# Kernel optimization log

Hardware: AMD Instinct MI355X
Metric: run time of the kernel (lower is better)

Reference implementation:

```python
import jax, jax.numpy as jnp
import numpy as np

HIDDEN = 1024
HEADS = 16
HEAD_DIM = HIDDEN // HEADS  # 64; softmax scale uses head_dim per SeqAttention(hidden_size=head_dim)


def setup_inputs() -> dict:
    key = jax.random.key(0)
    ks = jax.random.split(key, 7)
    B, M = 2, 2048
    s = 1.0 / np.sqrt(HIDDEN)
    return {
        "query": jax.random.normal(ks[0], (B, M, HIDDEN), jnp.float32),
        "key": jax.random.normal(ks[1], (B, M, HIDDEN), jnp.float32),
        "value": jax.random.normal(ks[2], (B, M, HIDDEN), jnp.float32),
        "Wq": jax.random.normal(ks[3], (HIDDEN, HIDDEN), jnp.float32) * s,
        "Wk": jax.random.normal(ks[4], (HIDDEN, HIDDEN), jnp.float32) * s,
        "Wv": jax.random.normal(ks[5], (HIDDEN, HIDDEN), jnp.float32) * s,
        "Wo": jax.random.normal(ks[6], (HIDDEN, HIDDEN), jnp.float32) * s,
    }


def _split_heads(x):
    # [B, T, H*D] -> [B, H, T, D]
    B, T, _ = x.shape
    return x.reshape(B, T, HEADS, HEAD_DIM).transpose(0, 2, 1, 3)


def reference(query, key, value, Wq, Wk, Wv, Wo):
    # nn.Linear(bias=False): y = x @ W.T
    q = _split_heads(query @ Wq.T)  # [B,H,M,D]
    k = _split_heads(key @ Wk.T)    # [B,H,N,D]
    v = _split_heads(value @ Wv.T)  # [B,H,N,D]
    scale = 1.0 / jnp.sqrt(jnp.asarray(HEAD_DIM, q.dtype))
    attn = jnp.einsum("bhmd,bhnd->bhmn", q, k) * scale
    attn = jax.nn.softmax(attn, axis=-1)
    out = jnp.einsum("bhmn,bhnd->bhmd", attn, v)  # [B,H,M,D]
    B, H, M, D = out.shape
    out = out.transpose(0, 2, 1, 3).reshape(B, M, H * D)
    return out @ Wo.T
```

## Files before the change

kernel.cpp:

```cpp
#include <hip/hip_runtime.h>

typedef __bf16 bf16;
typedef __bf16 bf16x2 __attribute__((ext_vector_type(2)));
typedef __bf16 bf16x8 __attribute__((ext_vector_type(8)));
typedef float  f32x4  __attribute__((ext_vector_type(4)));
typedef float  f32x16 __attribute__((ext_vector_type(16)));
typedef unsigned int u32;
typedef unsigned int u32x4 __attribute__((ext_vector_type(4)));

typedef __attribute__((address_space(1))) unsigned int gu32;
typedef __attribute__((address_space(3))) unsigned int lu32;

__device__ __forceinline__ void llds16(const void* g, void* l) {
  __builtin_amdgcn_global_load_lds((gu32*)g, (lu32*)l, 16, 0, 0);
}

__device__ __forceinline__ void cvt8(const float* __restrict__ src,
                                     bf16* __restrict__ dst, int i) {
  const float4* s4 = (const float4*)src;
  float4 a = s4[i * 2 + 0];
  float4 c = s4[i * 2 + 1];
  bf16x8 o;
  o[0] = (bf16)a.x; o[1] = (bf16)a.y; o[2] = (bf16)a.z; o[3] = (bf16)a.w;
  o[4] = (bf16)c.x; o[5] = (bf16)c.y; o[6] = (bf16)c.z; o[7] = (bf16)c.w;
  ((bf16x8*)dst)[i] = o;
}

__global__ __launch_bounds__(256) void cvt_bf16(const float* __restrict__ src,
                                                bf16* __restrict__ dst, int n8) {
  int i = blockIdx.x * blockDim.x + threadIdx.x;
  if (i < n8) cvt8(src, dst, i);
}

__global__ __launch_bounds__(256) void cvt_all(const float* __restrict__ w0,
                                               const float* __restrict__ w1,
                                               const float* __restrict__ w2,
                                               const float* __restrict__ w3,
                                               const float* __restrict__ x0,
                                               const float* __restrict__ x1,
                                               const float* __restrict__ x2,
                                               bf16* __restrict__ wdst,
                                               bf16* __restrict__ xdst) {
  const int b = blockIdx.x;
  if (b < 2048) {
    const int which = b >> 9;
    const float* src = (which == 0) ? w0 : (which == 1) ? w1 : (which == 2) ? w2 : w3;
    const int i = (b & 511) * 256 + threadIdx.x;
    cvt8(src, wdst + (size_t)which * (1u << 20), i);
  } else {
    const int b2 = b - 2048;
    const int which = b2 >> 11;
    const float* src = (which == 0) ? x0 : (which == 1) ? x1 : x2;
    const int i = (b2 & 2047) * 256 + threadIdx.x;
    cvt8(src, xdst + (size_t)which * (4u << 20), i);
  }
}

__global__ __launch_bounds__(256) void gemm_qkv(const bf16* __restrict__ A0,
                                                const bf16* __restrict__ A1,
                                                const bf16* __restrict__ A2,
                                                const bf16* __restrict__ Wb,
                                                bf16* __restrict__ qb,
                                                bf16* __restrict__ kb,
                                                bf16* __restrict__ vb,
                                                int zoff) {
  constexpr int K = 1024, BM = 128, BN = 128, BK = 32, NT = K / BK;
  __shared__ bf16 Alds[2][BM * BK];
  __shared__ bf16 Blds[2][BN * BK];
  const int t = threadIdx.x, w = t >> 6, l = t & 63;
  const int lr = l & 15, lg = l >> 4;
  const int bm = blockIdx.x * BM, bn = blockIdx.y * BN;
  const int z = blockIdx.z + zoff;
  const bf16* A = (z == 0) ? A0 : (z == 1) ? A1 : A2;
  const bf16* W = Wb + (size_t)z * (1u << 20);
  const int wm = (w >> 1) * 64, wn = (w & 1) * 64;

  f32x4 acc[4][4] = {};

  auto stage = [&](int buf, int kt) {
    const int k0 = kt * BK;
#pragma unroll
    for (int i = 0; i < 2; ++i) {
      int idx = i * 256 + t;
      int row = idx >> 2, kb2 = (idx & 3) * 16;
      llds16((const char*)A + ((size_t)(bm + row) * K + k0) * 2 + kb2,
             (char*)(&Alds[buf][0]) + (i * 4 + w) * 1024);
    }
#pragma unroll
    for (int i = 0; i < 2; ++i) {
      int idx = i * 256 + t;
      int row = idx >> 2, kb2 = (idx & 3) * 16;
      llds16((const char*)W + ((size_t)(bn + row) * K + k0) * 2 + kb2,
             (char*)(&Blds[buf][0]) + (i * 4 + w) * 1024);
    }
  };

  stage(0, 0);
  for (int kt = 0; kt < NT; ++kt) {
    __syncthreads();
    if (kt + 1 < NT) stage((kt + 1) & 1, kt + 1);
    const int cur = kt & 1;
    bf16x8 af[4], bfr[4];
#pragma unroll
    for (int i = 0; i < 4; ++i)
      af[i] = *(const bf16x8*)(&Alds[cur][(wm + i * 16 + lr) * BK + lg * 8]);
#pragma unroll
    for (int j = 0; j < 4; ++j)
      bfr[j] = *(const bf16x8*)(&Blds[cur][(wn + j * 16 + lr) * BK + lg * 8]);
    __builtin_amdgcn_s_setprio(1);
#pragma unroll
    for (int i = 0; i < 4; ++i)
#pragma unroll
      for (int j = 0; j < 4; ++j)
        acc[i][j] = __builtin_amdgcn_mfma_f32_16x16x32_bf16(af[i], bfr[j], acc[i][j], 0, 0, 0);
    __builtin_amdgcn_s_setprio(0);
  }

  bf16* Cout = (z == 0) ? qb : (z == 1) ? kb : vb;
  const float osc = (z == 0) ? 0.1803368801f : 1.0f;
#pragma unroll
  for (int i = 0; i < 4; ++i) {
#pragma unroll
    for (int j = 0; j < 4; ++j) {
#pragma unroll
      for (int r = 0; r < 4; ++r) {
        const int gm = bm + wm + i * 16 + lg * 4 + r;
        const int n  = bn + wn + j * 16 + lr;
        const int b = gm >> 11, m = gm & 2047;
        const int h = n >> 6, d = n & 63;
        const size_t off = (z < 2)
            ? ((size_t)((b * 16 + h) * 2048 + m) * 64 + d)
            : ((size_t)((b * 16 + h) * 64 + d) * 2048 + m);
        Cout[off] = (bf16)(acc[i][j][r] * osc);
      }
    }
  }
}

__global__ __launch_bounds__(256) void gemm_out(const bf16* __restrict__ A,
                                                const bf16* __restrict__ Bw,
                                                float* __restrict__ Cout) {
  constexpr int N = 1024, K = 1024;
  constexpr int BM = 128, BN = 64, BK = 32;
  __shared__ bf16 Alds[2][BM * BK];
  __shared__ bf16 Blds[2][BN * BK];
  const int t = threadIdx.x;
  const int w = t >> 6, l = t & 63;
  const int lr = l & 15, lg = l >> 4;
  const int bm = blockIdx.x * BM, bn = blockIdx.y * BN;
  const int wm = (w >> 1) * 64, wn = (w & 1) * 32;

  f32x4 acc[4][2] = {};

  auto stage = [&](int buf, int kt) {
    const int k0 = kt * BK;
#pragma unroll
    for (int i = 0; i < 2; ++i) {
      int idx = i * 256 + t;
      int row = idx >> 2, kb = (idx & 3) * 16;
      const char* g = (const char*)A + ((size_t)(bm + row) * K + k0) * 2 + kb;
      llds16(g, (char*)(&Alds[buf][0]) + (i * 4 + w) * 1024);
    }
    {
      int row = t >> 2, kb = (t & 3) * 16;
      const char* g = (const char*)Bw + ((size_t)(bn + row) * K + k0) * 2 + kb;
      llds16(g, (char*)(&Blds[buf][0]) + w * 1024);
    }
  };

  stage(0, 0);
  constexpr int NT = K / BK;
  for (int kt = 0; kt < NT; ++kt) {
    __syncthreads();
    if (kt + 1 < NT) stage((kt + 1) & 1, kt + 1);
    const int cur = kt & 1;
    bf16x8 af[4], bfr[2];
#pragma unroll
    for (int i = 0; i < 4; ++i)
      af[i] = *(const bf16x8*)(&Alds[cur][(wm + i * 16 + lr) * BK + lg * 8]);
#pragma unroll
    for (int j = 0; j < 2; ++j)
      bfr[j] = *(const bf16x8*)(&Blds[cur][(wn + j * 16 + lr) * BK + lg * 8]);
    __builtin_amdgcn_s_setprio(1);
#pragma unroll
    for (int i = 0; i < 4; ++i)
#pragma unroll
      for (int j = 0; j < 2; ++j)
        acc[i][j] = __builtin_amdgcn_mfma_f32_16x16x32_bf16(af[i], bfr[j], acc[i][j], 0, 0, 0);
    __builtin_amdgcn_s_setprio(0);
  }

#pragma unroll
  for (int i = 0; i < 4; ++i)
#pragma unroll
    for (int j = 0; j < 2; ++j)
#pragma unroll
      for (int r = 0; r < 4; ++r) {
        const int gm = bm + wm + i * 16 + lg * 4 + r;
        const int n  = bn + wn + j * 16 + lr;
        Cout[(size_t)gm * N + n] = acc[i][j][r];
      }
}

__global__ __launch_bounds__(256) void attn_fwd(const bf16* __restrict__ Qb,
                                                const bf16* __restrict__ Kb,
                                                const bf16* __restrict__ Vt,
                                                bf16* __restrict__ Out) {
  constexpr int Mlen = 2048, KVB = 64, NTT = Mlen / KVB;
  __shared__ bf16 Klds[3][KVB * 64];
  __shared__ bf16 Vlds[3][64 * KVB];
  const int t = threadIdx.x, w = t >> 6, l = t & 63;
  const int l31 = l & 31, hi = l >> 5;
  const int orig = blockIdx.x;
  const int wg = (orig & 7) * 64 + (orig >> 3);
  const int bh = wg >> 4;
  const int qr = (wg & 15) * 128 + w * 32;
  const int key = (l31 & 7) << 4;

  const bf16* qbase = Qb + ((size_t)bh * Mlen + qr + l31) * 64;
  bf16x8 qf[4];
#pragma unroll
  for (int dks = 0; dks < 4; ++dks)
    qf[dks] = *(const bf16x8*)(qbase + dks * 16 + hi * 8);

  f32x16 acco0 = {}, acco1 = {};
  float lsum = 0.f;

  const char* kTile0 = (const char*)Kb + (size_t)bh * Mlen * 64 * 2;
  const char* vBase  = (const char*)Vt + (size_t)bh * 64 * Mlen * 2;

  auto stageKV = [&](int buf, int tile) {
    const int kv0 = tile * KVB;
#pragma unroll
    for (int i = 0; i < 2; ++i) {
      int idx = i * 256 + t;
      int L = idx * 16;
      int row = L >> 7;
      int inner = (L & 127) ^ ((row & 7) << 4);
      llds16(kTile0 + (size_t)(kv0 + row) * 128 + inner,
             (char*)(&Klds[buf][0]) + (i * 4 + w) * 1024);
    }
#pragma unroll
    for (int i = 0; i < 2; ++i) {
      int idx = i * 256 + t;
      int L = idx * 16;
      int d = L >> 7;
      int inner = (L & 127) ^ ((d & 7) << 4);
      llds16(vBase + (size_t)d * (Mlen * 2) + kv0 * 2 + inner,
             (char*)(&Vlds[buf][0]) + (i * 4 + w) * 1024);
    }
  };

  stageKV(0, 0);
  int bufc = 0;
  for (int tile = 0; tile < NTT; ++tile) {
    const int bufn = (bufc == 2) ? 0 : bufc + 1;
    if (tile + 1 < NTT) {
      stageKV(bufn, tile + 1);
      asm volatile("s_waitcnt vmcnt(4)" ::: "memory");
    } else {
      asm volatile("s_waitcnt vmcnt(0)" ::: "memory");
    }
    __builtin_amdgcn_s_barrier();
    __builtin_amdgcn_sched_barrier(0);
    const char* kb_ = (const char*)(&Klds[bufc][0]);
    const char* vb_ = (const char*)(&Vlds[bufc][0]);

    f32x16 s0 = {}, s1 = {};
    __builtin_amdgcn_s_setprio(1);
#pragma unroll
    for (int dks = 0; dks < 4; ++dks) {
      const int a0 = (0 * 32 + l31) * 128 + ((dks * 32 + hi * 16) ^ key);
      const int a1 = (1 * 32 + l31) * 128 + ((dks * 32 + hi * 16) ^ key);
      bf16x8 kf0 = *(const bf16x8*)(kb_ + a0);
      bf16x8 kf1 = *(const bf16x8*)(kb_ + a1);
      s0 = __builtin_amdgcn_mfma_f32_32x32x16_bf16(kf0, qf[dks], s0, 0, 0, 0);
      s1 = __builtin_amdgcn_mfma_f32_32x32x16_bf16(kf1, qf[dks], s1, 0, 0, 0);
    }
    __builtin_amdgcn_s_setprio(0);

    u32 wrd0[8], wrd1[8];
    float ts = 0.f;
#pragma unroll
    for (int e2 = 0; e2 < 8; ++e2) {
      const float p00 = __builtin_amdgcn_exp2f(s0[2 * e2]);
      const float p01 = __builtin_amdgcn_exp2f(s0[2 * e2 + 1]);
      const float p10 = __builtin_amdgcn_exp2f(s1[2 * e2]);
      const float p11 = __builtin_amdgcn_exp2f(s1[2 * e2 + 1]);
      ts += (p00 + p01) + (p10 + p11);
      bf16x2 k0; k0[0] = (bf16)p00; k0[1] = (bf16)p01;
      bf16x2 k1; k1[0] = (bf16)p10; k1[1] = (bf16)p11;
      wrd0[e2] = __builtin_bit_cast(u32, k0);
      wrd1[e2] = __builtin_bit_cast(u32, k1);
    }
    lsum += ts;

    __builtin_amdgcn_s_setprio(1);
#pragma unroll
    for (int ks = 0; ks < 2; ++ks) {
      auto sa0 = __builtin_amdgcn_permlane32_swap(wrd0[4 * ks + 0], wrd0[4 * ks + 2], false, false);
      auto sa1 = __builtin_amdgcn_permlane32_swap(wrd0[4 * ks + 1], wrd0[4 * ks + 3], false, false);
      auto sb0 = __builtin_amdgcn_permlane32_swap(wrd1[4 * ks + 0], wrd1[4 * ks + 2], false, false);
      auto sb1 = __builtin_amdgcn_permlane32_swap(wrd1[4 * ks + 1], wrd1[4 * ks + 3], false, false);
      u32x4 fa, fb;
      fa[0] = (u32)sa0[0]; fa[1] = (u32)sa1[0]; fa[2] = (u32)sa0[1]; fa[3] = (u32)sa1[1];
      fb[0] = (u32)sb0[0]; fb[1] = (u32)sb1[0]; fb[2] = (u32)sb0[1]; fb[3] = (u32)sb1[1];
      const bf16x8 pa = __builtin_bit_cast(bf16x8, fa);
      const bf16x8 pb = __builtin_bit_cast(bf16x8, fb);
      const int c0 = (ks * 32 + hi * 16);
      bf16x8 va0 = *(const bf16x8*)(vb_ + (0 * 32 + l31) * 128 + ((0 * 64 + c0) ^ key));
      bf16x8 va1 = *(const bf16x8*)(vb_ + (1 * 32 + l31) * 128 + ((0 * 64 + c0) ^ key));
      bf16x8 vb0 = *(const bf16x8*)(vb_ + (0 * 32 + l31) * 128 + ((1 * 64 + c0) ^ key));
      bf16x8 vb1 = *(const bf16x8*)(vb_ + (1 * 32 + l31) * 128 + ((1 * 64 + c0) ^ key));
      acco0 = __builtin_amdgcn_mfma_f32_32x32x16_bf16(pa, va0, acco0, 0, 0, 0);
      acco1 = __builtin_amdgcn_mfma_f32_32x32x16_bf16(pa, va1, acco1, 0, 0, 0);
      acco0 = __builtin_amdgcn_mfma_f32_32x32x16_bf16(pb, vb0, acco0, 0, 0, 0);
      acco1 = __builtin_amdgcn_mfma_f32_32x32x16_bf16(pb, vb1, acco1, 0, 0, 0);
    }
    __builtin_amdgcn_s_setprio(0);
    bufc = bufn;
  }

  float lf = lsum + __shfl_xor(lsum, 32, 64);
  const float inv = 1.0f / lf;
  const int b = bh >> 4, h = bh & 15;
#pragma unroll
  for (int e = 0; e < 16; ++e) {
    const int ql = (e & 3) + 8 * (e >> 2) + 4 * hi;
    const float iv = __shfl(inv, ql, 64);
    const size_t row = (size_t)(b * 2048 + qr + ql) * 1024 + h * 64;
    Out[row + l31]      = (bf16)(acco0[e] * iv);
    Out[row + 32 + l31] = (bf16)(acco1[e] * iv);
  }
}

extern "C" void kernel_launch(void* const* d_in, const int* in_sizes, int n_in,
                              void* d_out, int out_size, void* d_ws, size_t ws_size,
                              hipStream_t stream) {
  const float* q  = (const float*)d_in[0];
  const float* k  = (const float*)d_in[1];
  const float* v  = (const float*)d_in[2];
  const float* Wq = (const float*)d_in[3];
  const float* Wk = (const float*)d_in[4];
  const float* Wv = (const float*)d_in[5];
  const float* Wo = (const float*)d_in[6];

  char* ws = (char*)d_ws;
  const dim3 cb(256);

  if (ws_size >= ((size_t)56 << 20)) {
    bf16* Wb = (bf16*)ws;
    bf16* Xq = (bf16*)(ws + (8u  << 20));
    bf16* Xk = (bf16*)(ws + (16u << 20));
    bf16* Xv = (bf16*)(ws + (24u << 20));
    bf16* qb = (bf16*)(ws + (32u << 20));
    bf16* kb = (bf16*)(ws + (40u << 20));
    bf16* vb = (bf16*)(ws + (48u << 20));
    bf16* Xa = (bf16*)(ws + (8u  << 20));

    cvt_all<<<8192, cb, 0, stream>>>(Wq, Wk, Wv, Wo, q, k, v, Wb, Xq);
    gemm_qkv<<<dim3(32, 8, 3), cb, 0, stream>>>(Xq, Xk, Xv, Wb, qb, kb, vb, 0);
    attn_fwd<<<512, cb, 0, stream>>>(qb, kb, vb, Xa);
    gemm_out<<<dim3(32, 16), cb, 0, stream>>>(Xa, Wb + 3 * (1u << 20), (float*)d_out);
  } else {
    bf16* Wb = (bf16*)ws;
    bf16* X  = (bf16*)(ws + (8u  << 20));
    bf16* qb = (bf16*)(ws + (16u << 20));
    bf16* kb = (bf16*)(ws + (24u << 20));
    bf16* vb = (bf16*)(ws + (32u << 20));
    bf16* Xa = (bf16*)(ws + (8u  << 20));

    cvt_all<<<2048, cb, 0, stream>>>(Wq, Wk, Wv, Wo, q, k, v, Wb, Wb);
    cvt_bf16<<<2048, cb, 0, stream>>>(q, X, 524288);
    gemm_qkv<<<dim3(32, 8, 1), cb, 0, stream>>>(X, X, X, Wb, qb, kb, vb, 0);
    cvt_bf16<<<2048, cb, 0, stream>>>(k, X, 524288);
    gemm_qkv<<<dim3(32, 8, 1), cb, 0, stream>>>(X, X, X, Wb, qb, kb, vb, 1);
    cvt_bf16<<<2048, cb, 0, stream>>>(v, X, 524288);
    gemm_qkv<<<dim3(32, 8, 1), cb, 0, stream>>>(X, X, X, Wb, qb, kb, vb, 2);
    attn_fwd<<<512, cb, 0, stream>>>(qb, kb, vb, Xa);
    gemm_out<<<dim3(32, 16), cb, 0, stream>>>(Xa, Wb + 3 * (1u << 20), (float*)d_out);
  }
}
```

Measured before the change: 131.8 us.

## Pre-swizzle V into MFMA fragment layout and load from global, row sums via MFMA

```diff
diff --git a/kernel.cpp b/kernel.cpp
--- a/kernel.cpp
+++ b/kernel.cpp
@@ -128,9 +128,17 @@
         const int n  = bn + wn + j * 16 + lr;
         const int b = gm >> 11, m = gm & 2047;
         const int h = n >> 6, d = n & 63;
-        const size_t off = (z < 2)
-            ? ((size_t)((b * 16 + h) * 2048 + m) * 64 + d)
-            : ((size_t)((b * 16 + h) * 64 + d) * 2048 + m);
+        size_t off;
+        if (z < 2) {
+          off = (size_t)((b * 16 + h) * 2048 + m) * 64 + d;
+        } else {
+          const int tile = m >> 6, kvb = (m >> 5) & 1, kss = (m >> 4) & 1;
+          const int hii = (m >> 3) & 1, jj = m & 7;
+          const int vblk = d >> 5, dl = d & 31;
+          off = (size_t)(b * 16 + h) * 131072 +
+                (size_t)(((tile * 4 + kvb * 2 + kss) * 2 + vblk) * 512 +
+                         (hii * 32 + dl) * 8 + jj);
+        }
         Cout[off] = (bf16)(acc[i][j][r] * osc);
       }
     }
@@ -207,8 +215,7 @@
                                                 const bf16* __restrict__ Vt,
                                                 bf16* __restrict__ Out) {
   constexpr int Mlen = 2048, KVB = 64, NTT = Mlen / KVB;
-  __shared__ bf16 Klds[3][KVB * 64];
-  __shared__ bf16 Vlds[3][64 * KVB];
+  __shared__ bf16 Klds[2][KVB * 64];
   const int t = threadIdx.x, w = t >> 6, l = t & 63;
   const int l31 = l & 31, hi = l >> 5;
   const int orig = blockIdx.x;
@@ -223,13 +230,18 @@
   for (int dks = 0; dks < 4; ++dks)
     qf[dks] = *(const bf16x8*)(qbase + dks * 16 + hi * 8);
 
+  u32x4 onesw;
+  onesw[0] = 0x3F803F80u; onesw[1] = 0x3F803F80u;
+  onesw[2] = 0x3F803F80u; onesw[3] = 0x3F803F80u;
+  const bf16x8 ones = __builtin_bit_cast(bf16x8, onesw);
+
   f32x16 acco0 = {}, acco1 = {};
-  float lsum = 0.f;
+  f32x16 accl = {};
 
   const char* kTile0 = (const char*)Kb + (size_t)bh * Mlen * 64 * 2;
-  const char* vBase  = (const char*)Vt + (size_t)bh * 64 * Mlen * 2;
-
-  auto stageKV = [&](int buf, int tile) {
+  const char* vBase  = (const char*)Vt + (size_t)bh * 131072 * 2;
+
+  auto stageK = [&](int buf, int tile) {
     const int kv0 = tile * KVB;
 #pragma unroll
     for (int i = 0; i < 2; ++i) {
@@ -240,31 +252,22 @@
       llds16(kTile0 + (size_t)(kv0 + row) * 128 + inner,
              (char*)(&Klds[buf][0]) + (i * 4 + w) * 1024);
     }
-#pragma unroll
-    for (int i = 0; i < 2; ++i) {
-      int idx = i * 256 + t;
-      int L = idx * 16;
-      int d = L >> 7;
-      int inner = (L & 127) ^ ((d & 7) << 4);
-      llds16(vBase + (size_t)d * (Mlen * 2) + kv0 * 2 + inner,
-             (char*)(&Vlds[buf][0]) + (i * 4 + w) * 1024);
-    }
   };
 
-  stageKV(0, 0);
-  int bufc = 0;
+  stageK(0, 0);
   for (int tile = 0; tile < NTT; ++tile) {
-    const int bufn = (bufc == 2) ? 0 : bufc + 1;
-    if (tile + 1 < NTT) {
-      stageKV(bufn, tile + 1);
-      asm volatile("s_waitcnt vmcnt(4)" ::: "memory");
-    } else {
-      asm volatile("s_waitcnt vmcnt(0)" ::: "memory");
-    }
-    __builtin_amdgcn_s_barrier();
-    __builtin_amdgcn_sched_barrier(0);
-    const char* kb_ = (const char*)(&Klds[bufc][0]);
-    const char* vb_ = (const char*)(&Vlds[bufc][0]);
+    __syncthreads();
+    const int cur = tile & 1;
+
+    const char* vTile = vBase + (size_t)tile * 8192;
+    bf16x8 vt[8];
+#pragma unroll
+    for (int bb = 0; bb < 8; ++bb)
+      vt[bb] = *(const bf16x8*)(vTile + bb * 1024 + l * 16);
+
+    if (tile + 1 < NTT) stageK(cur ^ 1, tile + 1);
+
+    const char* kb_ = (const char*)(&Klds[cur][0]);
 
     f32x16 s0 = {}, s1 = {};
     __builtin_amdgcn_s_setprio(1);
@@ -280,20 +283,17 @@
     __builtin_amdgcn_s_setprio(0);
 
     u32 wrd0[8], wrd1[8];
-    float ts = 0.f;
 #pragma unroll
     for (int e2 = 0; e2 < 8; ++e2) {
       const float p00 = __builtin_amdgcn_exp2f(s0[2 * e2]);
       const float p01 = __builtin_amdgcn_exp2f(s0[2 * e2 + 1]);
       const float p10 = __builtin_amdgcn_exp2f(s1[2 * e2]);
       const float p11 = __builtin_amdgcn_exp2f(s1[2 * e2 + 1]);
-      ts += (p00 + p01) + (p10 + p11);
       bf16x2 k0; k0[0] = (bf16)p00; k0[1] = (bf16)p01;
       bf16x2 k1; k1[0] = (bf16)p10; k1[1] = (bf16)p11;
       wrd0[e2] = __builtin_bit_cast(u32, k0);
       wrd1[e2] = __builtin_bit_cast(u32, k1);
     }
-    lsum += ts;
 
     __builtin_amdgcn_s_setprio(1);
 #pragma unroll
@@ -307,27 +307,21 @@
       fb[0] = (u32)sb0[0]; fb[1] = (u32)sb1[0]; fb[2] = (u32)sb0[1]; fb[3] = (u32)sb1[1];
       const bf16x8 pa = __builtin_bit_cast(bf16x8, fa);
       const bf16x8 pb = __builtin_bit_cast(bf16x8, fb);
-      const int c0 = (ks * 32 + hi * 16);
-      bf16x8 va0 = *(const bf16x8*)(vb_ + (0 * 32 + l31) * 128 + ((0 * 64 + c0) ^ key));
-      bf16x8 va1 = *(const bf16x8*)(vb_ + (1 * 32 + l31) * 128 + ((0 * 64 + c0) ^ key));
-      bf16x8 vb0 = *(const bf16x8*)(vb_ + (0 * 32 + l31) * 128 + ((1 * 64 + c0) ^ key));
-      bf16x8 vb1 = *(const bf16x8*)(vb_ + (1 * 32 + l31) * 128 + ((1 * 64 + c0) ^ key));
-      acco0 = __builtin_amdgcn_mfma_f32_32x32x16_bf16(pa, va0, acco0, 0, 0, 0);
-      acco1 = __builtin_amdgcn_mfma_f32_32x32x16_bf16(pa, va1, acco1, 0, 0, 0);
-      acco0 = __builtin_amdgcn_mfma_f32_32x32x16_bf16(pb, vb0, acco0, 0, 0, 0);
-      acco1 = __builtin_amdgcn_mfma_f32_32x32x16_bf16(pb, vb1, acco1, 0, 0, 0);
+      acco0 = __builtin_amdgcn_mfma_f32_32x32x16_bf16(pa, vt[ks * 2 + 0],     acco0, 0, 0, 0);
+      acco1 = __builtin_amdgcn_mfma_f32_32x32x16_bf16(pa, vt[ks * 2 + 1],     acco1, 0, 0, 0);
+      accl  = __builtin_amdgcn_mfma_f32_32x32x16_bf16(pa, ones,               accl,  0, 0, 0);
+      acco0 = __builtin_amdgcn_mfma_f32_32x32x16_bf16(pb, vt[4 + ks * 2 + 0], acco0, 0, 0, 0);
+      acco1 = __builtin_amdgcn_mfma_f32_32x32x16_bf16(pb, vt[4 + ks * 2 + 1], acco1, 0, 0, 0);
+      accl  = __builtin_amdgcn_mfma_f32_32x32x16_bf16(pb, ones,               accl,  0, 0, 0);
     }
     __builtin_amdgcn_s_setprio(0);
-    bufc = bufn;
-  }
-
-  float lf = lsum + __shfl_xor(lsum, 32, 64);
-  const float inv = 1.0f / lf;
+  }
+
   const int b = bh >> 4, h = bh & 15;
 #pragma unroll
   for (int e = 0; e < 16; ++e) {
     const int ql = (e & 3) + 8 * (e >> 2) + 4 * hi;
-    const float iv = __shfl(inv, ql, 64);
+    const float iv = 1.0f / accl[e];
     const size_t row = (size_t)(b * 2048 + qr + ql) * 1024 + h * 64;
     Out[row + l31]      = (bf16)(acco0[e] * iv);
     Out[row + 32 + l31] = (bf16)(acco1[e] * iv);
```

New measurement: 130.2 us. Within noise of the previous version (-1.2%).

## Software-pipeline QK and PV across tiles and compute row sums with MFMA

Applied to the files above, without the earlier changes.

```diff
diff --git a/kernel.cpp b/kernel.cpp
--- a/kernel.cpp
+++ b/kernel.cpp
@@ -207,8 +207,8 @@
                                                 const bf16* __restrict__ Vt,
                                                 bf16* __restrict__ Out) {
   constexpr int Mlen = 2048, KVB = 64, NTT = Mlen / KVB;
-  __shared__ bf16 Klds[3][KVB * 64];
-  __shared__ bf16 Vlds[3][64 * KVB];
+  __shared__ bf16 Klds[4][KVB * 64];
+  __shared__ bf16 Vlds[4][64 * KVB];
   const int t = threadIdx.x, w = t >> 6, l = t & 63;
   const int l31 = l & 31, hi = l >> 5;
   const int orig = blockIdx.x;
@@ -223,8 +223,13 @@
   for (int dks = 0; dks < 4; ++dks)
     qf[dks] = *(const bf16x8*)(qbase + dks * 16 + hi * 8);
 
+  u32x4 onesw;
+  onesw[0] = 0x3F803F80u; onesw[1] = 0x3F803F80u;
+  onesw[2] = 0x3F803F80u; onesw[3] = 0x3F803F80u;
+  const bf16x8 ones = __builtin_bit_cast(bf16x8, onesw);
+
   f32x16 acco0 = {}, acco1 = {};
-  float lsum = 0.f;
+  f32x16 accl = {};
 
   const char* kTile0 = (const char*)Kb + (size_t)bh * Mlen * 64 * 2;
   const char* vBase  = (const char*)Vt + (size_t)bh * 64 * Mlen * 2;
@@ -251,22 +256,18 @@
     }
   };
 
-  stageKV(0, 0);
-  int bufc = 0;
-  for (int tile = 0; tile < NTT; ++tile) {
-    const int bufn = (bufc == 2) ? 0 : bufc + 1;
+  auto STEP_HEAD = [&](int tile) {
     if (tile + 1 < NTT) {
-      stageKV(bufn, tile + 1);
+      stageKV((tile + 1) & 3, tile + 1);
       asm volatile("s_waitcnt vmcnt(4)" ::: "memory");
     } else {
       asm volatile("s_waitcnt vmcnt(0)" ::: "memory");
     }
     __builtin_amdgcn_s_barrier();
     __builtin_amdgcn_sched_barrier(0);
-    const char* kb_ = (const char*)(&Klds[bufc][0]);
-    const char* vb_ = (const char*)(&Vlds[bufc][0]);
-
-    f32x16 s0 = {}, s1 = {};
+  };
+  auto QK = [&](int tile, f32x16& s0, f32x16& s1) {
+    const char* kb_ = (const char*)(&Klds[tile & 3][0]);
     __builtin_amdgcn_s_setprio(1);
 #pragma unroll
     for (int dks = 0; dks < 4; ++dks) {
@@ -278,30 +279,29 @@
       s1 = __builtin_amdgcn_mfma_f32_32x32x16_bf16(kf1, qf[dks], s1, 0, 0, 0);
     }
     __builtin_amdgcn_s_setprio(0);
-
-    u32 wrd0[8], wrd1[8];
-    float ts = 0.f;
+  };
+  auto EXP = [&](const f32x16& s0, const f32x16& s1, u32 (&w0)[8], u32 (&w1)[8]) {
 #pragma unroll
     for (int e2 = 0; e2 < 8; ++e2) {
       const float p00 = __builtin_amdgcn_exp2f(s0[2 * e2]);
       const float p01 = __builtin_amdgcn_exp2f(s0[2 * e2 + 1]);
       const float p10 = __builtin_amdgcn_exp2f(s1[2 * e2]);
       const float p11 = __builtin_amdgcn_exp2f(s1[2 * e2 + 1]);
-      ts += (p00 + p01) + (p10 + p11);
       bf16x2 k0; k0[0] = (bf16)p00; k0[1] = (bf16)p01;
       bf16x2 k1; k1[0] = (bf16)p10; k1[1] = (bf16)p11;
-      wrd0[e2] = __builtin_bit_cast(u32, k0);
-      wrd1[e2] = __builtin_bit_cast(u32, k1);
-    }
-    lsum += ts;
-
+      w0[e2] = __builtin_bit_cast(u32, k0);
+      w1[e2] = __builtin_bit_cast(u32, k1);
+    }
+  };
+  auto PV = [&](int tprev, const u32 (&w0)[8], const u32 (&w1)[8]) {
+    const char* vb_ = (const char*)(&Vlds[tprev & 3][0]);
     __builtin_amdgcn_s_setprio(1);
 #pragma unroll
     for (int ks = 0; ks < 2; ++ks) {
-      auto sa0 = __builtin_amdgcn_permlane32_swap(wrd0[4 * ks + 0], wrd0[4 * ks + 2], false, false);
-      auto sa1 = __builtin_amdgcn_permlane32_swap(wrd0[4 * ks + 1], wrd0[4 * ks + 3], false, false);
-      auto sb0 = __builtin_amdgcn_permlane32_swap(wrd1[4 * ks + 0], wrd1[4 * ks + 2], false, false);
-      auto sb1 = __builtin_amdgcn_permlane32_swap(wrd1[4 * ks + 1], wrd1[4 * ks + 3], false, false);
+      auto sa0 = __builtin_amdgcn_permlane32_swap(w0[4 * ks + 0], w0[4 * ks + 2], false, false);
+      auto sa1 = __builtin_amdgcn_permlane32_swap(w0[4 * ks + 1], w0[4 * ks + 3], false, false);
+      auto sb0 = __builtin_amdgcn_permlane32_swap(w1[4 * ks + 0], w1[4 * ks + 2], false, false);
+      auto sb1 = __builtin_amdgcn_permlane32_swap(w1[4 * ks + 1], w1[4 * ks + 3], false, false);
       u32x4 fa, fb;
       fa[0] = (u32)sa0[0]; fa[1] = (u32)sa1[0]; fa[2] = (u32)sa0[1]; fa[3] = (u32)sa1[1];
       fb[0] = (u32)sb0[0]; fb[1] = (u32)sb1[0]; fb[2] = (u32)sb0[1]; fb[3] = (u32)sb1[1];
@@ -314,20 +314,48 @@
       bf16x8 vb1 = *(const bf16x8*)(vb_ + (1 * 32 + l31) * 128 + ((1 * 64 + c0) ^ key));
       acco0 = __builtin_amdgcn_mfma_f32_32x32x16_bf16(pa, va0, acco0, 0, 0, 0);
       acco1 = __builtin_amdgcn_mfma_f32_32x32x16_bf16(pa, va1, acco1, 0, 0, 0);
+      accl  = __builtin_amdgcn_mfma_f32_32x32x16_bf16(pa, ones, accl, 0, 0, 0);
       acco0 = __builtin_amdgcn_mfma_f32_32x32x16_bf16(pb, vb0, acco0, 0, 0, 0);
       acco1 = __builtin_amdgcn_mfma_f32_32x32x16_bf16(pb, vb1, acco1, 0, 0, 0);
+      accl  = __builtin_amdgcn_mfma_f32_32x32x16_bf16(pb, ones, accl, 0, 0, 0);
     }
     __builtin_amdgcn_s_setprio(0);
-    bufc = bufn;
-  }
-
-  float lf = lsum + __shfl_xor(lsum, 32, 64);
-  const float inv = 1.0f / lf;
+  };
+
+  u32 wE0[8], wE1[8], wO0[8], wO1[8];
+  f32x16 s0, s1;
+
+  stageKV(0, 0);
+  STEP_HEAD(0);
+  s0 = f32x16{}; s1 = f32x16{};
+  QK(0, s0, s1);
+  EXP(s0, s1, wE0, wE1);
+  for (int tp = 0; tp < 15; ++tp) {
+    const int to = 2 * tp + 1;
+    STEP_HEAD(to);
+    s0 = f32x16{}; s1 = f32x16{};
+    QK(to, s0, s1);
+    PV(to - 1, wE0, wE1);
+    EXP(s0, s1, wO0, wO1);
+    const int te = to + 1;
+    STEP_HEAD(te);
+    s0 = f32x16{}; s1 = f32x16{};
+    QK(te, s0, s1);
+    PV(te - 1, wO0, wO1);
+    EXP(s0, s1, wE0, wE1);
+  }
+  STEP_HEAD(31);
+  s0 = f32x16{}; s1 = f32x16{};
+  QK(31, s0, s1);
+  PV(30, wE0, wE1);
+  EXP(s0, s1, wO0, wO1);
+  PV(31, wO0, wO1);
+
   const int b = bh >> 4, h = bh & 15;
 #pragma unroll
   for (int e = 0; e < 16; ++e) {
     const int ql = (e & 3) + 8 * (e >> 2) + 4 * hi;
-    const float iv = __shfl(inv, ql, 64);
+    const float iv = 1.0f / accl[e];
     const size_t row = (size_t)(b * 2048 + qr + ql) * 1024 + h * 64;
     Out[row + l31]      = (bf16)(acco0[e] * iv);
     Out[row + 32 + l31] = (bf16)(acco1[e] * iv);
```

Measured after the change: 126.0 us. -4.4%, faster.
